# Kernel tuning notes

Hardware: AMD Instinct MI355X
Metric: run time of the kernel (lower is better)

The kernel has to match this reference:

```python
import jax, jax.numpy as jnp
import numpy as np

EMBED_DIM = 512
NUM_HEADS = 8
B, L_Q, L_K = 2, 2048, 2048


def setup_inputs() -> dict:
    key = jax.random.key(0)
    ks = jax.random.split(key, 8)
    s = 0.02  # weight init scale
    return {
        "query": jax.random.normal(ks[0], (B, L_Q, EMBED_DIM), jnp.float32),
        "key":   jax.random.normal(ks[1], (B, L_K, EMBED_DIM), jnp.float32),
        "value": jax.random.normal(ks[2], (B, L_K, EMBED_DIM), jnp.float32),
        "wq": jax.random.normal(ks[3], (EMBED_DIM, EMBED_DIM), jnp.float32) * s,
        "wk": jax.random.normal(ks[4], (EMBED_DIM, EMBED_DIM), jnp.float32) * s,
        "wv": jax.random.normal(ks[5], (EMBED_DIM, EMBED_DIM), jnp.float32) * s,
        "bq": jnp.zeros((EMBED_DIM,), jnp.float32),
        "bk": jnp.zeros((EMBED_DIM,), jnp.float32),
        "bv": jnp.zeros((EMBED_DIM,), jnp.float32),
        "wo": jax.random.normal(ks[6], (EMBED_DIM, EMBED_DIM), jnp.float32) * s,
        "bo": jnp.zeros((EMBED_DIM,), jnp.float32),
    }


def _prob_sparse_mask(query, key, num_heads):
    # Faithful to _prob_QK: max-mean sparsity score, top-k query selection,
    # gather of reduced queries, reduced QK matmul (vectorized, no python loops).
    Bq, Lq, D = query.shape
    Lk = key.shape[1]
    dh = D // num_heads
    n_top = int(np.log(Lk))  # int(np.ceil/np.log) as in source forward: int(np.log(L_K))
    Q = query.reshape(Bq, Lq, num_heads, dh)
    K = key.reshape(Bq, Lk, num_heads, dh)
    Qh = jnp.transpose(Q, (0, 2, 1, 3))                      # [B,H,Lq,dh]
    # NOTE: source does K.transpose(1,2).reshape(B,H,D,L_K) -- a reshape, not a
    # transpose of the last two dims. We replicate that exactly.
    Kr = jnp.transpose(K, (0, 2, 1, 3)).reshape(Bq, num_heads, dh, Lk)  # [B,H,dh,Lk]
    QK = jnp.einsum('bhqd,bhdk->bhqk', Qh, Kr)               # [B,H,Lq,Lk]
    M = QK.max(-1) - QK.sum(-1) / Lk                         # max-mean score [B,H,Lq]
    _, M_top = jax.lax.top_k(M, n_top)                       # [B,H,n_top]
    Q_red = jnp.take_along_axis(Qh, M_top[..., None], axis=2)  # [B,H,n_top,dh]
    QK_red = jnp.einsum('bhtd,bhdk->bhtk', Q_red, Kr)        # [B,H,n_top,Lk]
    # Scatter reduced rows back into a full additive attn mask (zeros elsewhere).
    mask = jnp.zeros((Bq, num_heads, Lq, Lk), QK.dtype)
    bi = jnp.arange(Bq)[:, None, None]
    hi = jnp.arange(num_heads)[None, :, None]
    return mask.at[bi, hi, M_top].set(QK_red)


def reference(query, key, value, wq, wk, wv, bq, bk, bv, wo, bo):
    Bq, Lq, D = query.shape
    Lk = key.shape[1]
    H = NUM_HEADS
    dh = D // H
    mask = _prob_sparse_mask(query, key, H)                  # [B,H,Lq,Lk]
    q = (query @ wq.T + bq).reshape(Bq, Lq, H, dh).transpose(0, 2, 1, 3)
    k = (key @ wk.T + bk).reshape(Bq, Lk, H, dh).transpose(0, 2, 1, 3)
    v = (value @ wv.T + bv).reshape(Bq, Lk, H, dh).transpose(0, 2, 1, 3)
    scores = jnp.einsum('bhqd,bhkd->bhqk', q, k) * (dh ** -0.5) + mask
    attn = jax.nn.softmax(scores, axis=-1)                   # dropout inactive (eval)
    out = jnp.einsum('bhqk,bhkd->bhqd', attn, v)
    out = out.transpose(0, 2, 1, 3).reshape(Bq, Lq, D)
    return out @ wo.T + bo
```

## Files before the change

kernel.cpp:

```cpp
#include <hip/hip_runtime.h>
#include <type_traits>

#define DEV static __device__ __forceinline__

typedef short s16;
typedef __attribute__((ext_vector_type(8))) short short8;
typedef __attribute__((ext_vector_type(4))) float f32x4;
typedef __attribute__((ext_vector_type(16))) float f32x16;

#define NB 2
#define NH 8
#define SL 2048
#define DM 512
#define DH 64
#define NTOP 7
#define NCAND 16
#define LOG2E 1.4426950408889634f
#define NROWS (NB*NH*SL)
#define FSPLIT 4
#define SSPLIT 4

DEV short f2bf(float x){
  union { float f; unsigned u; } v; v.f = x;
  unsigned r = v.u + 0x7fffu + ((v.u >> 16) & 1u);
  return (short)(r >> 16);
}
DEV f32x4 mfma16(short8 a, short8 b, f32x4 c){
  return __builtin_amdgcn_mfma_f32_16x16x32_bf16(a, b, c, 0, 0, 0);
}
DEV f32x16 mfma32(short8 a, short8 b, f32x16 c){
  return __builtin_amdgcn_mfma_f32_32x32x16_bf16(a, b, c, 0, 0, 0);
}
DEV unsigned cvtpk(float lo, float hi){
  unsigned r;
  asm("v_cvt_pk_bf16_f32 %0, %1, %2" : "=v"(r) : "v"(lo), "v"(hi));
  return r;
}
DEV void gl2lds16(const s16* g, s16* l){
  __builtin_amdgcn_global_load_lds(
      (const __attribute__((address_space(1))) unsigned*)g,
      (__attribute__((address_space(3))) unsigned*)l, 16, 0, 0);
}

__global__ void prep_kernel(const float* __restrict__ query, const float* __restrict__ key,
    const float* __restrict__ value,
    const float* __restrict__ wq, const float* __restrict__ wk,
    const float* __restrict__ wv, const float* __restrict__ wo,
    s16* __restrict__ xq, s16* __restrict__ xk, s16* __restrict__ xv,
    s16* __restrict__ khat,
    s16* __restrict__ wqb, s16* __restrict__ wkb, s16* __restrict__ wvb, s16* __restrict__ wob){
  const int nbb = (NB*SL*DM)/256;
  const int wbb = (DM*DM)/256;
  __shared__ s16 thi[64][66];
  int bid = blockIdx.x;
  int t = threadIdx.x;
  if (bid < nbb){ int i = bid*256 + t; xq[i] = f2bf(query[i]); return; }
  bid -= nbb;
  if (bid < nbb){ int i = bid*256 + t; xk[i] = f2bf(key[i]); return; }
  bid -= nbb;
  if (bid < nbb){ int i = bid*256 + t; xv[i] = f2bf(value[i]); return; }
  bid -= nbb;
  if (bid < 512){
    int k6 = bid & 31, h = (bid >> 5) & 7, b = bid >> 8;
    int kl = t & 63, dq = t >> 6;
    #pragma unroll
    for (int dd = 0; dd < 16; ++dd){
      int d = dd*4 + dq;
      thi[d][kl] = f2bf(key[((size_t)b*SL + d*32 + k6)*DM + h*DH + kl]);
    }
    __syncthreads();
    int d2 = t & 63, kq = t >> 6;
    size_t obase = (((size_t)(b*NH + h))*SL + (size_t)k6*64)*DH;
    #pragma unroll
    for (int kk = 0; kk < 16; ++kk){
      int kl2 = kk*4 + kq;
      khat[obase + (size_t)kl2*DH + d2] = thi[d2][kl2];
    }
    return;
  }
  bid -= 512;
  if (bid < wbb){ int i = bid*256 + t; wqb[i] = f2bf(wq[i]); return; }
  bid -= wbb;
  if (bid < wbb){ int i = bid*256 + t; wkb[i] = f2bf(wk[i]); return; }
  bid -= wbb;
  if (bid < wbb){ int i = bid*256 + t; wvb[i] = f2bf(wv[i]); return; }
  bid -= wbb;
  if (bid < wbb){ int i = bid*256 + t; wob[i] = f2bf(wo[i]); return; }
}

__global__ __launch_bounds__(256) void vpt_kernel(const s16* __restrict__ Vp, s16* __restrict__ VpT){
  __shared__ s16 tl[64][66];
  int bid = blockIdx.x;
  int k6 = bid & 31, h = (bid >> 5) & 7, b = bid >> 8;
  int t = threadIdx.x;
  int d = t & 63, kq = t >> 6;
  #pragma unroll
  for (int kk = 0; kk < 16; ++kk){
    int kl = kk*4 + kq;
    tl[kl][d] = Vp[((size_t)b*SL + k6*64 + kl)*DM + h*DH + d];
  }
  __syncthreads();
  int kl2 = t & 63, dq = t >> 6;
  size_t obase = ((size_t)(b*NH + h))*DH*SL + (size_t)k6*64;
  #pragma unroll
  for (int dd = 0; dd < 16; ++dd){
    int d2 = dd*4 + dq;
    VpT[obase + (size_t)d2*SL + kl2] = tl[kl2][d2];
  }
}

template<int OUTF32>
DEV void gemm_body(const s16* __restrict__ A, const s16* __restrict__ Bw,
        const float* __restrict__ bias, void* __restrict__ Cout, int bid, int tid, float scale){
  __shared__ __align__(16) s16 Abuf[2][128*64];
  __shared__ __align__(16) s16 Bbuf[2][64*64];
  int nt = bid >> 3, ot = bid & 7;
  int w = tid >> 6, l = tid & 63;
  int lr = l & 15, lg = l >> 4;
  int n0 = nt*128, o0 = ot*64;
  auto stage = [&](int cur, int kg){
    #pragma unroll
    for (int i = 0; i < 4; ++i){
      int r = w*32 + i*8 + (l>>3);
      int cs = (l&7) ^ (r&7);
      gl2lds16(A + (size_t)(n0 + r)*DM + kg + cs*8, &Abuf[cur][(w*32 + i*8)*64]);
    }
    #pragma unroll
    for (int i = 0; i < 2; ++i){
      int r = w*16 + i*8 + (l>>3);
      int cs = (l&7) ^ (r&7);
      gl2lds16(Bw + (size_t)(o0 + r)*DM + kg + cs*8, &Bbuf[cur][(w*16 + i*8)*64]);
    }
  };
  f32x4 acc[2][4] = {};
  stage(0, 0);
  __syncthreads();
  const int NIT = DM/64;
  for (int it = 0; it < NIT; ++it){
    int cur = it & 1;
    if (it + 1 < NIT) stage(cur^1, (it+1)*64);
    #pragma unroll
    for (int kc = 0; kc < 2; ++kc){
      short8 a0 = *(const short8*)&Abuf[cur][(w*32 +      lr)*64 + ((kc*4+lg) ^ (lr&7))*8];
      short8 a1 = *(const short8*)&Abuf[cur][(w*32 + 16 + lr)*64 + ((kc*4+lg) ^ (lr&7))*8];
      #pragma unroll
      for (int c = 0; c < 4; ++c){
        short8 bf = *(const short8*)&Bbuf[cur][(c*16 + lr)*64 + ((kc*4+lg) ^ (lr&7))*8];
        acc[0][c] = mfma16(a0, bf, acc[0][c]);
        acc[1][c] = mfma16(a1, bf, acc[1][c]);
      }
    }
    __syncthreads();
  }
  #pragma unroll
  for (int sub = 0; sub < 2; ++sub)
    #pragma unroll
    for (int c = 0; c < 4; ++c){
      int col = o0 + c*16 + lr;
      float bb = bias[col];
      #pragma unroll
      for (int j = 0; j < 4; ++j){
        int row = n0 + w*32 + sub*16 + lg*4 + j;
        float v = (acc[sub][c][j] + bb)*scale;
        if (OUTF32) ((float*)Cout)[(size_t)row*DM + col] = v;
        else        ((s16*) Cout)[(size_t)row*DM + col] = f2bf(v);
      }
    }
}

__global__ __launch_bounds__(256) void gemm_proj(const s16* __restrict__ Aq, const s16* __restrict__ Ak,
        const s16* __restrict__ Av, const s16* __restrict__ Wq, const s16* __restrict__ Wk,
        const s16* __restrict__ Wv, const float* __restrict__ bq, const float* __restrict__ bk,
        const float* __restrict__ bv, s16* __restrict__ Oq, s16* __restrict__ Ok, s16* __restrict__ Ov){
  int which = blockIdx.x >> 8;
  const s16* A  = which == 0 ? Aq : which == 1 ? Ak : Av;
  const s16* Bw = which == 0 ? Wq : which == 1 ? Wk : Wv;
  const float* bias = which == 0 ? bq : which == 1 ? bk : bv;
  s16* C = which == 0 ? Oq : which == 1 ? Ok : Ov;
  float scale = which == 0 ? 0.125f*LOG2E : 1.0f;
  gemm_body<0>(A, Bw, bias, C, blockIdx.x & 255, threadIdx.x, scale);
}

__global__ __launch_bounds__(256) void gemm_out(const s16* __restrict__ A, const s16* __restrict__ Bw,
        const float* __restrict__ bias, float* __restrict__ Cout){
  gemm_body<1>(A, Bw, bias, Cout, blockIdx.x, threadIdx.x, 1.0f);
}

__global__ __launch_bounds__(512) void stats_kernel(const s16* __restrict__ xq,
        const s16* __restrict__ khat, float* __restrict__ Mmx, float* __restrict__ Msm){
  __shared__ __align__(16) s16 Hbuf[2][64*64];
  int bid = blockIdx.x;
  int s = bid & 3, qt = (bid >> 2) & 15, h = (bid >> 6) & 7, b = bid >> 9;
  int tid = threadIdx.x;
  int w = tid >> 6, l = tid & 63;
  int lr = l & 15, lg = l >> 4;
  int dx = lr & 7;
  int q0 = qt*128 + w*16;
  const s16* qp = xq + ((size_t)b*SL + q0 + lr)*DM + h*DH + lg*8;
  short8 qh0 = *(const short8*)qp;
  short8 qh1 = *(const short8*)(qp + 32);
  const s16* kb = khat + ((size_t)b*NH + h)*SL*DH;
  const s16* hR0 = &Hbuf[0][lr*64 + ((lg      ^ dx)*8)];
  const s16* hR1 = &Hbuf[0][lr*64 + (((4+lg) ^ dx)*8)];
  int rS = tid >> 3;
  int slot = tid & 7;
  int cs = slot ^ (rS & 7);
  int kbeg = s*(SL/SSPLIT);
  const int NT = (SL/SSPLIT)/64;
  f32x4 hreg;
  auto loadr = [&](int t){
    hreg = *(const f32x4*)(kb + (size_t)(kbeg + t*64 + rS)*DH + cs*8);
  };
  auto writer = [&](int buf){
    *(f32x4*)&Hbuf[buf][rS*64 + slot*8] = hreg;
  };
  float mx = -1e30f, sm = 0.f;
  auto body = [&](auto CURC){
    constexpr int CUR = decltype(CURC)::value;
    #pragma unroll
    for (int t = 0; t < 4; ++t){
      short8 kh0 = *(const short8*)(hR0 + CUR*4096 + t*1024);
      short8 kh1 = *(const short8*)(hR1 + CUR*4096 + t*1024);
      f32x4 sacc = {};
      sacc = mfma16(kh0, qh0, sacc);
      sacc = mfma16(kh1, qh1, sacc);
      #pragma unroll
      for (int j = 0; j < 4; ++j){ mx = fmaxf(mx, sacc[j]); sm += sacc[j]; }
    }
  };
  loadr(0);
  writer(0);
  loadr(1);
  __syncthreads();
  auto step = [&](auto TC){
    constexpr int T = decltype(TC)::value;
    if constexpr (T + 1 < NT) writer((T+1)&1);
    if constexpr (T + 2 < NT) loadr(T+2);
    body(std::integral_constant<int, T&1>{});
    __syncthreads();
  };
  step(std::integral_constant<int,0>{}); step(std::integral_constant<int,1>{});
  step(std::integral_constant<int,2>{}); step(std::integral_constant<int,3>{});
  step(std::integral_constant<int,4>{}); step(std::integral_constant<int,5>{});
  step(std::integral_constant<int,6>{}); step(std::integral_constant<int,7>{});
  mx = fmaxf(mx, __shfl_xor(mx, 16));
  mx = fmaxf(mx, __shfl_xor(mx, 32));
  sm += __shfl_xor(sm, 16);
  sm += __shfl_xor(sm, 32);
  if (lg == 0){
    size_t row = ((size_t)b*NH + h)*SL + q0 + lr;
    Mmx[(size_t)s*NROWS + row] = mx;
    Msm[(size_t)s*NROWS + row] = sm;
  }
}

__global__ __launch_bounds__(256) void topk_kernel(const float* __restrict__ Mmx,
        const float* __restrict__ Msm, int* __restrict__ candidx, int* __restrict__ rowsel){
  int bh = blockIdx.x;
  int t = threadIdx.x;
  int w = t >> 6, l = t & 63;
  __shared__ float smv[SL];
  __shared__ float rv[4];
  __shared__ int   ri[4];
  size_t base = (size_t)bh*SL;
  for (int i = t; i < SL; i += 256){
    float mx = Mmx[base + i];
    float sm = Msm[base + i];
    #pragma unroll
    for (int s = 1; s < SSPLIT; ++s){
      mx = fmaxf(mx, Mmx[(size_t)s*NROWS + base + i]);
      sm += Msm[(size_t)s*NROWS + base + i];
    }
    smv[i] = mx - sm*(1.0f/SL);
    rowsel[base + i] = -1;
  }
  __syncthreads();
  for (int tt = 0; tt < NCAND; ++tt){
    float bvv = -1e38f; int bi = SL;
    for (int i = t; i < SL; i += 256){
      float v = smv[i];
      if (v > bvv){ bvv = v; bi = i; }
    }
    #pragma unroll
    for (int off = 32; off >= 1; off >>= 1){
      float ov = __shfl_xor(bvv, off);
      int oi = __shfl_xor(bi, off);
      if (ov > bvv || (ov == bvv && oi < bi)){ bvv = ov; bi = oi; }
    }
    if (l == 0){ rv[w] = bvv; ri[w] = bi; }
    __syncthreads();
    if (t == 0){
      float bv2 = rv[0]; int bi2 = ri[0];
      #pragma unroll
      for (int ww = 1; ww < 4; ++ww)
        if (rv[ww] > bv2 || (rv[ww] == bv2 && ri[ww] < bi2)){ bv2 = rv[ww]; bi2 = ri[ww]; }
      candidx[bh*NCAND + tt] = bi2;
      smv[bi2] = -1e38f;
    }
    __syncthreads();
  }
}

__global__ __launch_bounds__(256) void cand_kernel(const float* __restrict__ query,
        const float* __restrict__ key, const int* __restrict__ candidx,
        float* __restrict__ candrows, float* __restrict__ cmx, float* __restrict__ csm){
  __shared__ float tile[64][65];
  __shared__ float qs[NCAND][64];
  int bid = blockIdx.x;
  int k6 = bid & 31, h = (bid >> 5) & 7, b = bid >> 8;
  int bh = b*NH + h;
  int t = threadIdx.x;
  int kl = t & 63, w = t >> 6;
  for (int i = t; i < NCAND*64; i += 256){
    int tt = i >> 6, d = i & 63;
    qs[tt][d] = query[((size_t)b*SL + candidx[bh*NCAND + tt])*DM + h*DH + d];
  }
  #pragma unroll
  for (int dd = 0; dd < 16; ++dd){
    int d = dd*4 + w;
    tile[d][kl] = key[((size_t)b*SL + d*32 + k6)*DM + h*DH + kl];
  }
  __syncthreads();
  for (int tt = w; tt < NCAND; tt += 4){
    float acc = 0.f;
    #pragma unroll
    for (int d = 0; d < 64; ++d)
      acc = fmaf(qs[tt][d], tile[d][kl], acc);
    candrows[((size_t)bh*NCAND + tt)*SL + k6*64 + kl] = acc*LOG2E;
    float mx = acc, sm = acc;
    #pragma unroll
    for (int off = 1; off < 64; off <<= 1){
      mx = fmaxf(mx, __shfl_xor(mx, off));
      sm += __shfl_xor(sm, off);
    }
    if (kl == 0){
      cmx[((size_t)bh*NCAND + tt)*32 + k6] = mx;
      csm[((size_t)bh*NCAND + tt)*32 + k6] = sm;
    }
  }
}

__global__ __launch_bounds__(64) void topsel_kernel(const float* __restrict__ cmx,
        const float* __restrict__ csm, const int* __restrict__ candidx, int* __restrict__ rowsel){
  int bh = blockIdx.x;
  int l = threadIdx.x;
  __shared__ float Mex[NCAND];
  if (l < NCAND){
    float mx = -1e38f, sm = 0.f;
    #pragma unroll 4
    for (int p = 0; p < 32; ++p){
      mx = fmaxf(mx, cmx[((size_t)bh*NCAND + l)*32 + p]);
      sm += csm[((size_t)bh*NCAND + l)*32 + p];
    }
    Mex[l] = mx - sm*(1.0f/SL);
  }
  __syncthreads();
  if (l == 0){
    unsigned used = 0;
    for (int tt = 0; tt < NTOP; ++tt){
      float bv = -1e38f; int bslot = 0; int brow = 1 << 30;
      for (int c = 0; c < NCAND; ++c){
        if (used & (1u << c)) continue;
        int row = candidx[bh*NCAND + c];
        float v = Mex[c];
        if (v > bv || (v == bv && row < brow)){ bv = v; bslot = c; brow = row; }
      }
      used |= 1u << bslot;
      rowsel[(size_t)bh*SL + brow] = bslot;
    }
  }
}

__global__ __launch_bounds__(256, 3) void flash_kernel(const s16* __restrict__ Qp,
        const s16* __restrict__ Kp, const s16* __restrict__ VpT,
        const float* __restrict__ candrows, const int* __restrict__ rowsel,
        float* __restrict__ Opart, float* __restrict__ lpart){
  __shared__ __align__(16) s16 SB[4*64*64];
  int bid = blockIdx.x;
  int s = bid & 3, qt = (bid >> 2) & 15, h = (bid >> 6) & 7, b = bid >> 9;
  int tid = threadIdx.x;
  int w = tid >> 6, l = tid & 63;
  int ln = l & 31, lh = l >> 5;
  int q0 = qt*128 + w*32;
  int bh = b*NH + h;
  const s16* qp = Qp + ((size_t)b*SL + q0 + ln)*DM + h*DH + lh*8;
  short8 bq[4];
  #pragma unroll
  for (int kc = 0; kc < 4; ++kc) bq[kc] = *(const short8*)(qp + kc*16);
  int sel = rowsel[(size_t)bh*SL + q0 + ln];
  const float* mrow = candrows + ((size_t)bh*NCAND + (sel >= 0 ? sel : 0))*SL;
  const s16* kpb = Kp + (size_t)b*SL*DM + h*DH;
  const s16* vtb = VpT + (size_t)bh*DH*SL;
  const s16* kR[2][4];
  #pragma unroll
  for (int g = 0; g < 2; ++g)
    #pragma unroll
    for (int kc = 0; kc < 4; ++kc)
      kR[g][kc] = &SB[(g*32 + ln)*64 + ((((kc*2 + lh) ^ (ln & 7) ^ ((ln >> 3) & 3))*8))];
  int r8 = l >> 3;
  int slot = l & 7;
  int cs = slot ^ r8 ^ w;
  int kbeg = s*(SL/FSPLIT);
  const int NT = (SL/FSPLIT)/64;
  f32x4 kreg[2], vreg[2];
  auto loadr = [&](int t){
    int kg = kbeg + t*64;
    #pragma unroll
    for (int c = 0; c < 2; ++c){
      int r = c*32 + w*8 + r8;
      kreg[c] = *(const f32x4*)(kpb + (size_t)(kg + r)*DM + cs*8);
      vreg[c] = *(const f32x4*)(vtb + (size_t)r*SL + kg + cs*8);
    }
  };
  auto writer = [&](int buf){
    #pragma unroll
    for (int c = 0; c < 2; ++c){
      int r = c*32 + w*8 + r8;
      *(f32x4*)&SB[(size_t)buf*4096 + r*64 + slot*8] = kreg[c];
      *(f32x4*)&SB[8192 + (size_t)buf*4096 + r*64 + slot*8] = vreg[c];
    }
  };
  short8 ones;
  #pragma unroll
  for (int i = 0; i < 8; ++i) ones[i] = (short)0x3F80;
  f32x16 accO[2] = {};
  f32x16 accL = {};
  auto body = [&](auto CURC, int k0){
    constexpr int CB = decltype(CURC)::value * 8192;
    f32x16 S[2] = {};
    __builtin_amdgcn_s_setprio(1);
    #pragma unroll
    for (int g = 0; g < 2; ++g)
      #pragma unroll
      for (int kc = 0; kc < 4; ++kc){
        short8 kf = *(const short8*)((const char*)kR[g][kc] + CB);
        S[g] = mfma32(kf, bq[kc], S[g]);
      }
    __builtin_amdgcn_s_setprio(0);
    if (sel >= 0){
      #pragma unroll
      for (int g = 0; g < 2; ++g)
        #pragma unroll
        for (int rq = 0; rq < 4; ++rq)
          #pragma unroll
          for (int j = 0; j < 4; ++j)
            S[g][rq*4 + j] += mrow[k0 + g*32 + rq*8 + lh*4 + j];
    }
    #pragma unroll
    for (int g = 0; g < 2; ++g)
      #pragma unroll
      for (int e = 0; e < 16; ++e)
        S[g][e] = exp2f(S[g][e]);
    unsigned W[2][8];
    #pragma unroll
    for (int g = 0; g < 2; ++g)
      #pragma unroll
      for (int t = 0; t < 8; ++t)
        W[g][t] = cvtpk(S[g][2*t], S[g][2*t+1]);
    short8 pf[4];
    #pragma unroll
    for (int kc = 0; kc < 4; ++kc){
      int g = kc >> 1, j = kc & 1;
      unsigned a0 = W[g][4*j + 0], a1 = W[g][4*j + 2];
      asm("v_permlane32_swap_b32 %0, %1" : "+v"(a0), "+v"(a1));
      unsigned b0 = W[g][4*j + 1], b1 = W[g][4*j + 3];
      asm("v_permlane32_swap_b32 %0, %1" : "+v"(b0), "+v"(b1));
      union { unsigned u[4]; short8 s8; } uu;
      uu.u[0] = a0; uu.u[1] = b0; uu.u[2] = a1; uu.u[3] = b1;
      pf[kc] = uu.s8;
    }
    __builtin_amdgcn_s_setprio(1);
    #pragma unroll
    for (int kc = 0; kc < 4; ++kc)
      accL = mfma32(ones, pf[kc], accL);
    #pragma unroll
    for (int dg = 0; dg < 2; ++dg)
      #pragma unroll
      for (int kc = 0; kc < 4; ++kc){
        short8 vf = *(const short8*)((const char*)kR[dg][kc] + CB + 16384);
        accO[dg] = mfma32(vf, pf[kc], accO[dg]);
      }
    __builtin_amdgcn_s_setprio(0);
  };
  loadr(0);
  writer(0);
  loadr(1);
  __syncthreads();
  auto step = [&](auto TC){
    constexpr int T = decltype(TC)::value;
    if constexpr (T + 1 < NT) writer((T+1)&1);
    if constexpr (T + 2 < NT) loadr(T+2);
    body(std::integral_constant<int, T&1>{}, kbeg + T*64);
    __syncthreads();
  };
  step(std::integral_constant<int,0>{}); step(std::integral_constant<int,1>{});
  step(std::integral_constant<int,2>{}); step(std::integral_constant<int,3>{});
  step(std::integral_constant<int,4>{}); step(std::integral_constant<int,5>{});
  step(std::integral_constant<int,6>{}); step(std::integral_constant<int,7>{});
  size_t row = (size_t)bh*SL + q0 + ln;
  float* Op = Opart + ((size_t)s*NROWS + row)*DH;
  #pragma unroll
  for (int dg = 0; dg < 2; ++dg)
    #pragma unroll
    for (int rq = 0; rq < 4; ++rq){
      f32x4 v = { accO[dg][rq*4+0], accO[dg][rq*4+1], accO[dg][rq*4+2], accO[dg][rq*4+3] };
      *(f32x4*)(Op + dg*32 + rq*8 + lh*4) = v;
    }
  if (lh == 0)
    lpart[(size_t)s*NROWS + row] = accL[0];
}

__global__ __launch_bounds__(256) void flash_combine(const float* __restrict__ Opart,
        const float* __restrict__ lpart, s16* __restrict__ outh){
  int row = blockIdx.x*4 + (threadIdx.x >> 6);
  int d = threadIdx.x & 63;
  float L = 0.f, o = 0.f;
  #pragma unroll
  for (int s = 0; s < FSPLIT; ++s){
    L += lpart[(size_t)s*NROWS + row];
    o += Opart[((size_t)s*NROWS + row)*DH + d];
  }
  o /= L;
  int b = row >> 14, h = (row >> 11) & 7, q = row & (SL - 1);
  outh[((size_t)b*SL + q)*DM + h*DH + d] = f2bf(o);
}

extern "C" void kernel_launch(void* const* d_in, const int* in_sizes, int n_in,
                              void* d_out, int out_size, void* d_ws, size_t ws_size,
                              hipStream_t stream){
  (void)in_sizes; (void)n_in; (void)out_size;
  const float* query = (const float*)d_in[0];
  const float* key   = (const float*)d_in[1];
  const float* value = (const float*)d_in[2];
  const float* wq    = (const float*)d_in[3];
  const float* wk    = (const float*)d_in[4];
  const float* wv    = (const float*)d_in[5];
  const float* bq    = (const float*)d_in[6];
  const float* bk    = (const float*)d_in[7];
  const float* bv    = (const float*)d_in[8];
  const float* wo    = (const float*)d_in[9];
  const float* bo    = (const float*)d_in[10];

  const size_t NE = (size_t)NB*SL*DM;
  const size_t WE = (size_t)DM*DM;

  char* p = (char*)d_ws;
  size_t off = 0;
  auto alloc = [&](size_t n)->char*{ char* r = p + off; off += (n + 255) & ~(size_t)255; return r; };
  s16* wob = (s16*)alloc(WE*2);
  s16* Qp  = (s16*)alloc(NE*2);
  s16* Kp  = (s16*)alloc(NE*2);
  s16* VpT = (s16*)alloc(NE*2);
  float* candrows = (float*)alloc((size_t)NB*NH*NCAND*SL*4);
  int* candidx  = (int*)alloc((size_t)NB*NH*NCAND*4);
  float* cmx    = (float*)alloc((size_t)NB*NH*NCAND*32*4);
  float* csm    = (float*)alloc((size_t)NB*NH*NCAND*32*4);
  int* rowsel   = (int*)alloc((size_t)NROWS*4);
  float* Mmx    = (float*)alloc((size_t)SSPLIT*NROWS*4);
  float* Msm    = (float*)alloc((size_t)SSPLIT*NROWS*4);
  float* lpart  = (float*)alloc((size_t)FSPLIT*NROWS*4);
  float* Opart  = (float*)alloc((size_t)FSPLIT*NROWS*DH*4);
  s16* outh = (s16*)alloc(NE*2);
  s16* xq   = (s16*)alloc(NE*2);
  s16* xk   = (s16*)alloc(NE*2);
  s16* xv   = (s16*)alloc(NE*2);
  s16* khat = (s16*)alloc(NE*2);
  s16* wqb = (s16*)alloc(WE*2);
  s16* wkb = (s16*)alloc(WE*2);
  s16* wvb = (s16*)alloc(WE*2);
  s16* Vp  = (s16*)alloc(NE*2);
  if (off > ws_size) return;

  const int nbb = (int)(NE/256);
  const int wbb = (int)(WE/256);
  prep_kernel<<<3*nbb + 512 + 4*wbb, 256, 0, stream>>>(query, key, value, wq, wk, wv, wo,
      xq, xk, xv, khat, wqb, wkb, wvb, wob);

  gemm_proj<<<3*256, 256, 0, stream>>>(xq, xk, xv, wqb, wkb, wvb, bq, bk, bv, Qp, Kp, Vp);
  vpt_kernel<<<512, 256, 0, stream>>>(Vp, VpT);

  stats_kernel<<<NB*NH*(SL/128)*SSPLIT, 512, 0, stream>>>(xq, khat, Mmx, Msm);
  topk_kernel<<<NB*NH, 256, 0, stream>>>(Mmx, Msm, candidx, rowsel);
  cand_kernel<<<512, 256, 0, stream>>>(query, key, candidx, candrows, cmx, csm);
  topsel_kernel<<<NB*NH, 64, 0, stream>>>(cmx, csm, candidx, rowsel);

  flash_kernel<<<NB*NH*(SL/128)*FSPLIT, 256, 0, stream>>>(Qp, Kp, VpT, candrows, rowsel,
      Opart, lpart);
  flash_combine<<<NROWS/4, 256, 0, stream>>>(Opart, lpart, outh);
  gemm_out<<<256, 256, 0, stream>>>(outh, wob, bo, (float*)d_out);
}
```

Before: 149.2 us.

## Fuse fp32-to-bf16 conversion into GEMMs and flash combine into output GEMM

Removes the separate conversion pass for inputs and weights. The projection GEMM and the stats kernel now read fp32 directly and pack to bf16 in registers, staging through registers into LDS instead of direct global-to-LDS loads. The flash split combine and normalization move into the output GEMM's A-operand load, which drops a kernel and the bf16 intermediate buffer. The top-k candidate search keeps per-thread scores in registers and rescans only on the winning thread, replacing the LDS array scan. In exchange the GEMMs read twice the bytes per element and the output GEMM recomputes the combine for each of its 8 column tiles.

```diff
diff --git a/kernel.cpp b/kernel.cpp
--- a/kernel.cpp
+++ b/kernel.cpp
@@ -36,56 +36,35 @@
   asm("v_cvt_pk_bf16_f32 %0, %1, %2" : "=v"(r) : "v"(lo), "v"(hi));
   return r;
 }
-DEV void gl2lds16(const s16* g, s16* l){
-  __builtin_amdgcn_global_load_lds(
-      (const __attribute__((address_space(1))) unsigned*)g,
-      (__attribute__((address_space(3))) unsigned*)l, 16, 0, 0);
-}
-
-__global__ void prep_kernel(const float* __restrict__ query, const float* __restrict__ key,
-    const float* __restrict__ value,
-    const float* __restrict__ wq, const float* __restrict__ wk,
-    const float* __restrict__ wv, const float* __restrict__ wo,
-    s16* __restrict__ xq, s16* __restrict__ xk, s16* __restrict__ xv,
-    s16* __restrict__ khat,
-    s16* __restrict__ wqb, s16* __restrict__ wkb, s16* __restrict__ wvb, s16* __restrict__ wob){
-  const int nbb = (NB*SL*DM)/256;
-  const int wbb = (DM*DM)/256;
+DEV short8 pack8(f32x4 x0, f32x4 x1){
+  union { unsigned u[4]; short8 s8; } uu;
+  uu.u[0] = cvtpk(x0[0], x0[1]);
+  uu.u[1] = cvtpk(x0[2], x0[3]);
+  uu.u[2] = cvtpk(x1[0], x1[1]);
+  uu.u[3] = cvtpk(x1[2], x1[3]);
+  return uu.s8;
+}
+
+__global__ __launch_bounds__(256) void prep_kernel(const float* __restrict__ key,
+        s16* __restrict__ khat){
   __shared__ s16 thi[64][66];
   int bid = blockIdx.x;
   int t = threadIdx.x;
-  if (bid < nbb){ int i = bid*256 + t; xq[i] = f2bf(query[i]); return; }
-  bid -= nbb;
-  if (bid < nbb){ int i = bid*256 + t; xk[i] = f2bf(key[i]); return; }
-  bid -= nbb;
-  if (bid < nbb){ int i = bid*256 + t; xv[i] = f2bf(value[i]); return; }
-  bid -= nbb;
-  if (bid < 512){
-    int k6 = bid & 31, h = (bid >> 5) & 7, b = bid >> 8;
-    int kl = t & 63, dq = t >> 6;
-    #pragma unroll
-    for (int dd = 0; dd < 16; ++dd){
-      int d = dd*4 + dq;
-      thi[d][kl] = f2bf(key[((size_t)b*SL + d*32 + k6)*DM + h*DH + kl]);
-    }
-    __syncthreads();
-    int d2 = t & 63, kq = t >> 6;
-    size_t obase = (((size_t)(b*NH + h))*SL + (size_t)k6*64)*DH;
-    #pragma unroll
-    for (int kk = 0; kk < 16; ++kk){
-      int kl2 = kk*4 + kq;
-      khat[obase + (size_t)kl2*DH + d2] = thi[d2][kl2];
-    }
-    return;
-  }
-  bid -= 512;
-  if (bid < wbb){ int i = bid*256 + t; wqb[i] = f2bf(wq[i]); return; }
-  bid -= wbb;
-  if (bid < wbb){ int i = bid*256 + t; wkb[i] = f2bf(wk[i]); return; }
-  bid -= wbb;
-  if (bid < wbb){ int i = bid*256 + t; wvb[i] = f2bf(wv[i]); return; }
-  bid -= wbb;
-  if (bid < wbb){ int i = bid*256 + t; wob[i] = f2bf(wo[i]); return; }
+  int k6 = bid & 31, h = (bid >> 5) & 7, b = bid >> 8;
+  int kl = t & 63, dq = t >> 6;
+  #pragma unroll
+  for (int dd = 0; dd < 16; ++dd){
+    int d = dd*4 + dq;
+    thi[d][kl] = f2bf(key[((size_t)b*SL + d*32 + k6)*DM + h*DH + kl]);
+  }
+  __syncthreads();
+  int d2 = t & 63, kq = t >> 6;
+  size_t obase = (((size_t)(b*NH + h))*SL + (size_t)k6*64)*DH;
+  #pragma unroll
+  for (int kk = 0; kk < 16; ++kk){
+    int kl2 = kk*4 + kq;
+    khat[obase + (size_t)kl2*DH + d2] = thi[d2][kl2];
+  }
 }
 
 __global__ __launch_bounds__(256) void vpt_kernel(const s16* __restrict__ Vp, s16* __restrict__ VpT){
@@ -109,49 +88,79 @@
   }
 }
 
-template<int OUTF32>
-DEV void gemm_body(const s16* __restrict__ A, const s16* __restrict__ Bw,
-        const float* __restrict__ bias, void* __restrict__ Cout, int bid, int tid, float scale){
+DEV void gemm_inner(const s16* __restrict__ Ab, const s16* __restrict__ Bb,
+        f32x4 acc[2][4], int w, int lr, int lg){
+  #pragma unroll
+  for (int kc = 0; kc < 2; ++kc){
+    short8 a0 = *(const short8*)&Ab[(w*32 +      lr)*64 + ((kc*4+lg) ^ (lr&7))*8];
+    short8 a1 = *(const short8*)&Ab[(w*32 + 16 + lr)*64 + ((kc*4+lg) ^ (lr&7))*8];
+    #pragma unroll
+    for (int c = 0; c < 4; ++c){
+      short8 bf = *(const short8*)&Bb[(c*16 + lr)*64 + ((kc*4+lg) ^ (lr&7))*8];
+      acc[0][c] = mfma16(a0, bf, acc[0][c]);
+      acc[1][c] = mfma16(a1, bf, acc[1][c]);
+    }
+  }
+}
+
+__global__ __launch_bounds__(256) void gemm_proj(const float* __restrict__ Aq,
+        const float* __restrict__ Ak, const float* __restrict__ Av,
+        const float* __restrict__ Wq, const float* __restrict__ Wk, const float* __restrict__ Wv,
+        const float* __restrict__ bq, const float* __restrict__ bk, const float* __restrict__ bv,
+        s16* __restrict__ Oq, s16* __restrict__ Ok, s16* __restrict__ Ov){
   __shared__ __align__(16) s16 Abuf[2][128*64];
   __shared__ __align__(16) s16 Bbuf[2][64*64];
+  int which = blockIdx.x >> 8;
+  const float* A  = which == 0 ? Aq : which == 1 ? Ak : Av;
+  const float* Bw = which == 0 ? Wq : which == 1 ? Wk : Wv;
+  const float* bias = which == 0 ? bq : which == 1 ? bk : bv;
+  s16* C = which == 0 ? Oq : which == 1 ? Ok : Ov;
+  float scale = which == 0 ? 0.125f*LOG2E : 1.0f;
+  int bid = blockIdx.x & 255;
   int nt = bid >> 3, ot = bid & 7;
+  int tid = threadIdx.x;
   int w = tid >> 6, l = tid & 63;
   int lr = l & 15, lg = l >> 4;
   int n0 = nt*128, o0 = ot*64;
-  auto stage = [&](int cur, int kg){
+  int r8 = l >> 3, slot = l & 7;
+  int cs = slot ^ r8;
+  short8 areg[4], breg[2];
+  auto loadr = [&](int kg){
     #pragma unroll
     for (int i = 0; i < 4; ++i){
-      int r = w*32 + i*8 + (l>>3);
-      int cs = (l&7) ^ (r&7);
-      gl2lds16(A + (size_t)(n0 + r)*DM + kg + cs*8, &Abuf[cur][(w*32 + i*8)*64]);
+      const float* p = A + (size_t)(n0 + w*32 + i*8 + r8)*DM + kg + cs*8;
+      areg[i] = pack8(*(const f32x4*)p, *(const f32x4*)(p + 4));
     }
     #pragma unroll
     for (int i = 0; i < 2; ++i){
-      int r = w*16 + i*8 + (l>>3);
-      int cs = (l&7) ^ (r&7);
-      gl2lds16(Bw + (size_t)(o0 + r)*DM + kg + cs*8, &Bbuf[cur][(w*16 + i*8)*64]);
-    }
+      const float* p = Bw + (size_t)(o0 + w*16 + i*8 + r8)*DM + kg + cs*8;
+      breg[i] = pack8(*(const f32x4*)p, *(const f32x4*)(p + 4));
+    }
+  };
+  auto writer = [&](int buf){
+    #pragma unroll
+    for (int i = 0; i < 4; ++i)
+      *(short8*)&Abuf[buf][(w*32 + i*8 + r8)*64 + slot*8] = areg[i];
+    #pragma unroll
+    for (int i = 0; i < 2; ++i)
+      *(short8*)&Bbuf[buf][(w*16 + i*8 + r8)*64 + slot*8] = breg[i];
   };
   f32x4 acc[2][4] = {};
-  stage(0, 0);
-  __syncthreads();
-  const int NIT = DM/64;
-  for (int it = 0; it < NIT; ++it){
-    int cur = it & 1;
-    if (it + 1 < NIT) stage(cur^1, (it+1)*64);
-    #pragma unroll
-    for (int kc = 0; kc < 2; ++kc){
-      short8 a0 = *(const short8*)&Abuf[cur][(w*32 +      lr)*64 + ((kc*4+lg) ^ (lr&7))*8];
-      short8 a1 = *(const short8*)&Abuf[cur][(w*32 + 16 + lr)*64 + ((kc*4+lg) ^ (lr&7))*8];
-      #pragma unroll
-      for (int c = 0; c < 4; ++c){
-        short8 bf = *(const short8*)&Bbuf[cur][(c*16 + lr)*64 + ((kc*4+lg) ^ (lr&7))*8];
-        acc[0][c] = mfma16(a0, bf, acc[0][c]);
-        acc[1][c] = mfma16(a1, bf, acc[1][c]);
-      }
-    }
+  loadr(0);
+  writer(0);
+  loadr(64);
+  __syncthreads();
+  auto step = [&](auto TC){
+    constexpr int T = decltype(TC)::value;
+    if constexpr (T + 1 < 8) writer((T+1)&1);
+    if constexpr (T + 2 < 8) loadr((T+2)*64);
+    gemm_inner(&Abuf[T&1][0], &Bbuf[T&1][0], acc, w, lr, lg);
     __syncthreads();
-  }
+  };
+  step(std::integral_constant<int,0>{}); step(std::integral_constant<int,1>{});
+  step(std::integral_constant<int,2>{}); step(std::integral_constant<int,3>{});
+  step(std::integral_constant<int,4>{}); step(std::integral_constant<int,5>{});
+  step(std::integral_constant<int,6>{}); step(std::integral_constant<int,7>{});
   #pragma unroll
   for (int sub = 0; sub < 2; ++sub)
     #pragma unroll
@@ -161,32 +170,90 @@
       #pragma unroll
       for (int j = 0; j < 4; ++j){
         int row = n0 + w*32 + sub*16 + lg*4 + j;
-        float v = (acc[sub][c][j] + bb)*scale;
-        if (OUTF32) ((float*)Cout)[(size_t)row*DM + col] = v;
-        else        ((s16*) Cout)[(size_t)row*DM + col] = f2bf(v);
+        C[(size_t)row*DM + col] = f2bf((acc[sub][c][j] + bb)*scale);
       }
     }
 }
 
-__global__ __launch_bounds__(256) void gemm_proj(const s16* __restrict__ Aq, const s16* __restrict__ Ak,
-        const s16* __restrict__ Av, const s16* __restrict__ Wq, const s16* __restrict__ Wk,
-        const s16* __restrict__ Wv, const float* __restrict__ bq, const float* __restrict__ bk,
-        const float* __restrict__ bv, s16* __restrict__ Oq, s16* __restrict__ Ok, s16* __restrict__ Ov){
-  int which = blockIdx.x >> 8;
-  const s16* A  = which == 0 ? Aq : which == 1 ? Ak : Av;
-  const s16* Bw = which == 0 ? Wq : which == 1 ? Wk : Wv;
-  const float* bias = which == 0 ? bq : which == 1 ? bk : bv;
-  s16* C = which == 0 ? Oq : which == 1 ? Ok : Ov;
-  float scale = which == 0 ? 0.125f*LOG2E : 1.0f;
-  gemm_body<0>(A, Bw, bias, C, blockIdx.x & 255, threadIdx.x, scale);
-}
-
-__global__ __launch_bounds__(256) void gemm_out(const s16* __restrict__ A, const s16* __restrict__ Bw,
-        const float* __restrict__ bias, float* __restrict__ Cout){
-  gemm_body<1>(A, Bw, bias, Cout, blockIdx.x, threadIdx.x, 1.0f);
-}
-
-__global__ __launch_bounds__(512) void stats_kernel(const s16* __restrict__ xq,
+__global__ __launch_bounds__(256) void gemm_out(const float* __restrict__ Opart,
+        const float* __restrict__ lpart, const float* __restrict__ Wo,
+        const float* __restrict__ bo, float* __restrict__ Cout){
+  __shared__ __align__(16) s16 Abuf[2][128*64];
+  __shared__ __align__(16) s16 Bbuf[2][64*64];
+  int bid = blockIdx.x;
+  int nt = bid >> 3, ot = bid & 7;
+  int tid = threadIdx.x;
+  int w = tid >> 6, l = tid & 63;
+  int lr = l & 15, lg = l >> 4;
+  int n0 = nt*128, o0 = ot*64;
+  int r8 = l >> 3, slot = l & 7;
+  int cs = slot ^ r8;
+  short8 areg[4], breg[2];
+  auto loadr = [&](int kg){
+    int h = kg >> 6;
+    int d0 = cs*8;
+    #pragma unroll
+    for (int i = 0; i < 4; ++i){
+      int row = n0 + w*32 + i*8 + r8;
+      int b = row >> 11, q = row & (SL - 1);
+      size_t idx = ((size_t)(b*NH + h))*SL + q;
+      float L = 0.f;
+      f32x4 a0 = {}, a1 = {};
+      #pragma unroll
+      for (int s = 0; s < FSPLIT; ++s){
+        L += lpart[(size_t)s*NROWS + idx];
+        const float* p = Opart + ((size_t)s*NROWS + idx)*DH + d0;
+        a0 += *(const f32x4*)p;
+        a1 += *(const f32x4*)(p + 4);
+      }
+      float rinv = 1.0f / L;
+      areg[i] = pack8(a0*rinv, a1*rinv);
+    }
+    #pragma unroll
+    for (int i = 0; i < 2; ++i){
+      const float* p = Wo + (size_t)(o0 + w*16 + i*8 + r8)*DM + kg + cs*8;
+      breg[i] = pack8(*(const f32x4*)p, *(const f32x4*)(p + 4));
+    }
+  };
+  auto writer = [&](int buf){
+    #pragma unroll
+    for (int i = 0; i < 4; ++i)
+      *(short8*)&Abuf[buf][(w*32 + i*8 + r8)*64 + slot*8] = areg[i];
+    #pragma unroll
+    for (int i = 0; i < 2; ++i)
+      *(short8*)&Bbuf[buf][(w*16 + i*8 + r8)*64 + slot*8] = breg[i];
+  };
+  f32x4 acc[2][4] = {};
+  loadr(0);
+  writer(0);
+  loadr(64);
+  __syncthreads();
+  auto step = [&](auto TC){
+    constexpr int T = decltype(TC)::value;
+    if constexpr (T + 1 < 8) writer((T+1)&1);
+    if constexpr (T + 2 < 8) loadr((T+2)*64);
+    gemm_inner(&Abuf[T&1][0], &Bbuf[T&1][0], acc, w, lr, lg);
+    __syncthreads();
+  };
+  step(std::integral_constant<int,0>{}); step(std::integral_constant<int,1>{});
+  step(std::integral_constant<int,2>{}); step(std::integral_constant<int,3>{});
+  step(std::integral_constant<int,4>{}); step(std::integral_constant<int,5>{});
+  step(std::integral_constant<int,6>{}); step(std::integral_constant<int,7>{});
+  #pragma unroll
+  for (int sub = 0; sub < 2; ++sub)
+    #pragma unroll
+    for (int c = 0; c < 4; ++c){
+      int col = o0 + c*16 + lr;
+      float bb = bo[col];
+      #pragma unroll
+      for (int j = 0; j < 4; ++j){
+        int row = n0 + w*32 + sub*16 + lg*4 + j;
+        Cout[(size_t)row*DM + col] = acc[sub][c][j] + bb;
+      }
+    }
+}
+
+__global__ __launch_bounds__(512) void stats_kernel(const float* __restrict__ query,
         const s16* __restrict__ khat, float* __restrict__ Mmx, float* __restrict__ Msm){
   __shared__ __align__(16) s16 Hbuf[2][64*64];
   int bid = blockIdx.x;
@@ -196,9 +263,9 @@
   int lr = l & 15, lg = l >> 4;
   int dx = lr & 7;
   int q0 = qt*128 + w*16;
-  const s16* qp = xq + ((size_t)b*SL + q0 + lr)*DM + h*DH + lg*8;
-  short8 qh0 = *(const short8*)qp;
-  short8 qh1 = *(const short8*)(qp + 32);
+  const float* qpf = query + ((size_t)b*SL + q0 + lr)*DM + h*DH + lg*8;
+  short8 qh0 = pack8(*(const f32x4*)qpf,        *(const f32x4*)(qpf + 4));
+  short8 qh1 = pack8(*(const f32x4*)(qpf + 32), *(const f32x4*)(qpf + 36));
   const s16* kb = khat + ((size_t)b*NH + h)*SL*DH;
   const s16* hR0 = &Hbuf[0][lr*64 + ((lg      ^ dx)*8)];
   const s16* hR1 = &Hbuf[0][lr*64 + (((4+lg) ^ dx)*8)];
@@ -259,11 +326,14 @@
   int bh = blockIdx.x;
   int t = threadIdx.x;
   int w = t >> 6, l = t & 63;
-  __shared__ float smv[SL];
-  __shared__ float rv[4];
-  __shared__ int   ri[4];
+  __shared__ float bval[4];
+  __shared__ int   bidx[4];
+  __shared__ int   gsel;
   size_t base = (size_t)bh*SL;
-  for (int i = t; i < SL; i += 256){
+  float v[8];
+  #pragma unroll
+  for (int j = 0; j < 8; ++j){
+    int i = j*256 + t;
     float mx = Mmx[base + i];
     float sm = Msm[base + i];
     #pragma unroll
@@ -271,33 +341,40 @@
       mx = fmaxf(mx, Mmx[(size_t)s*NROWS + base + i]);
       sm += Msm[(size_t)s*NROWS + base + i];
     }
-    smv[i] = mx - sm*(1.0f/SL);
+    v[j] = mx - sm*(1.0f/SL);
     rowsel[base + i] = -1;
   }
-  __syncthreads();
+  float lv = -1e38f; int li = SL;
+  #pragma unroll
+  for (int j = 0; j < 8; ++j)
+    if (v[j] > lv){ lv = v[j]; li = j*256 + t; }
   for (int tt = 0; tt < NCAND; ++tt){
-    float bvv = -1e38f; int bi = SL;
-    for (int i = t; i < SL; i += 256){
-      float v = smv[i];
-      if (v > bvv){ bvv = v; bi = i; }
-    }
+    float cv = lv; int ci = li;
     #pragma unroll
     for (int off = 32; off >= 1; off >>= 1){
-      float ov = __shfl_xor(bvv, off);
-      int oi = __shfl_xor(bi, off);
-      if (ov > bvv || (ov == bvv && oi < bi)){ bvv = ov; bi = oi; }
-    }
-    if (l == 0){ rv[w] = bvv; ri[w] = bi; }
+      float ov = __shfl_xor(cv, off);
+      int oi = __shfl_xor(ci, off);
+      if (ov > cv || (ov == cv && oi < ci)){ cv = ov; ci = oi; }
+    }
+    if (l == 0){ bval[w] = cv; bidx[w] = ci; }
     __syncthreads();
     if (t == 0){
-      float bv2 = rv[0]; int bi2 = ri[0];
+      float bv2 = bval[0]; int bi2 = bidx[0];
       #pragma unroll
       for (int ww = 1; ww < 4; ++ww)
-        if (rv[ww] > bv2 || (rv[ww] == bv2 && ri[ww] < bi2)){ bv2 = rv[ww]; bi2 = ri[ww]; }
+        if (bval[ww] > bv2 || (bval[ww] == bv2 && bidx[ww] < bi2)){ bv2 = bval[ww]; bi2 = bidx[ww]; }
       candidx[bh*NCAND + tt] = bi2;
-      smv[bi2] = -1e38f;
+      gsel = bi2;
     }
     __syncthreads();
+    int win = gsel;
+    if ((win & 255) == t){
+      v[win >> 8] = -1e38f;
+      lv = -1e38f; li = SL;
+      #pragma unroll
+      for (int j = 0; j < 8; ++j)
+        if (v[j] > lv){ lv = v[j]; li = j*256 + t; }
+    }
   }
 }
 
@@ -508,21 +585,6 @@
     }
   if (lh == 0)
     lpart[(size_t)s*NROWS + row] = accL[0];
-}
-
-__global__ __launch_bounds__(256) void flash_combine(const float* __restrict__ Opart,
-        const float* __restrict__ lpart, s16* __restrict__ outh){
-  int row = blockIdx.x*4 + (threadIdx.x >> 6);
-  int d = threadIdx.x & 63;
-  float L = 0.f, o = 0.f;
-  #pragma unroll
-  for (int s = 0; s < FSPLIT; ++s){
-    L += lpart[(size_t)s*NROWS + row];
-    o += Opart[((size_t)s*NROWS + row)*DH + d];
-  }
-  o /= L;
-  int b = row >> 14, h = (row >> 11) & 7, q = row & (SL - 1);
-  outh[((size_t)b*SL + q)*DM + h*DH + d] = f2bf(o);
 }
 
 extern "C" void kernel_launch(void* const* d_in, const int* in_sizes, int n_in,
@@ -542,15 +604,15 @@
   const float* bo    = (const float*)d_in[10];
 
   const size_t NE = (size_t)NB*SL*DM;
-  const size_t WE = (size_t)DM*DM;
 
   char* p = (char*)d_ws;
   size_t off = 0;
   auto alloc = [&](size_t n)->char*{ char* r = p + off; off += (n + 255) & ~(size_t)255; return r; };
-  s16* wob = (s16*)alloc(WE*2);
   s16* Qp  = (s16*)alloc(NE*2);
   s16* Kp  = (s16*)alloc(NE*2);
+  s16* Vp  = (s16*)alloc(NE*2);
   s16* VpT = (s16*)alloc(NE*2);
+  s16* khat = (s16*)alloc(NE*2);
   float* candrows = (float*)alloc((size_t)NB*NH*NCAND*SL*4);
   int* candidx  = (int*)alloc((size_t)NB*NH*NCAND*4);
   float* cmx    = (float*)alloc((size_t)NB*NH*NCAND*32*4);
@@ -560,32 +622,18 @@
   float* Msm    = (float*)alloc((size_t)SSPLIT*NROWS*4);
   float* lpart  = (float*)alloc((size_t)FSPLIT*NROWS*4);
   float* Opart  = (float*)alloc((size_t)FSPLIT*NROWS*DH*4);
-  s16* outh = (s16*)alloc(NE*2);
-  s16* xq   = (s16*)alloc(NE*2);
-  s16* xk   = (s16*)alloc(NE*2);
-  s16* xv   = (s16*)alloc(NE*2);
-  s16* khat = (s16*)alloc(NE*2);
-  s16* wqb = (s16*)alloc(WE*2);
-  s16* wkb = (s16*)alloc(WE*2);
-  s16* wvb = (s16*)alloc(WE*2);
-  s16* Vp  = (s16*)alloc(NE*2);
   if (off > ws_size) return;
 
-  const int nbb = (int)(NE/256);
-  const int wbb = (int)(WE/256);
-  prep_kernel<<<3*nbb + 512 + 4*wbb, 256, 0, stream>>>(query, key, value, wq, wk, wv, wo,
-      xq, xk, xv, khat, wqb, wkb, wvb, wob);
-
-  gemm_proj<<<3*256, 256, 0, stream>>>(xq, xk, xv, wqb, wkb, wvb, bq, bk, bv, Qp, Kp, Vp);
+  prep_kernel<<<512, 256, 0, stream>>>(key, khat);
+  gemm_proj<<<3*256, 256, 0, stream>>>(query, key, value, wq, wk, wv, bq, bk, bv, Qp, Kp, Vp);
   vpt_kernel<<<512, 256, 0, stream>>>(Vp, VpT);
 
-  stats_kernel<<<NB*NH*(SL/128)*SSPLIT, 512, 0, stream>>>(xq, khat, Mmx, Msm);
+  stats_kernel<<<NB*NH*(SL/128)*SSPLIT, 512, 0, stream>>>(query, khat, Mmx, Msm);
   topk_kernel<<<NB*NH, 256, 0, stream>>>(Mmx, Msm, candidx, rowsel);
   cand_kernel<<<512, 256, 0, stream>>>(query, key, candidx, candrows, cmx, csm);
   topsel_kernel<<<NB*NH, 64, 0, stream>>>(cmx, csm, candidx, rowsel);
 
   flash_kernel<<<NB*NH*(SL/128)*FSPLIT, 256, 0, stream>>>(Qp, Kp, VpT, candrows, rowsel,
       Opart, lpart);
-  flash_combine<<<NROWS/4, 256, 0, stream>>>(Opart, lpart, outh);
-  gemm_out<<<256, 256, 0, stream>>>(outh, wob, bo, (float*)d_out);
-}
+  gemm_out<<<256, 256, 0, stream>>>(Opart, lpart, wo, bo, (float*)d_out);
+}
```

After: 204.5 us. 1.37x slower.
